# Optimization experiments

Measured on AMD Instinct MI355X. Metric: run time of the kernel, lower is better.

## Reference

```python
import jax, jax.numpy as jnp
import numpy as np

N, NFEAT, NFEAT_EXT, NHID, NCLASS, NHEADS = 8192, 512, 128, 256, 10, 8


def setup_inputs() -> dict:
    key = jax.random.key(0)
    ks = jax.random.split(key, 12)
    s = lambda fan_in: 1.0 / np.sqrt(fan_in)
    return {
        "x": jax.random.normal(ks[0], (N, NFEAT), jnp.float32),
        "adj": jax.random.uniform(ks[1], (N, N), jnp.float32) / N,  # row-stochastic-ish normalized adjacency
        "sub_fea": jax.random.normal(ks[2], (1, NFEAT_EXT), jnp.float32),
        # GraphConvolution 1: nfeat -> nhid
        "gc1_W": jax.random.normal(ks[3], (NFEAT, NHID), jnp.float32) * s(NFEAT),
        "gc1_b": jnp.zeros((NHID,), jnp.float32),
        # GraphConvolution 2: nhid -> 2*nhid
        "gc2_W": jax.random.normal(ks[4], (NHID, 2 * NHID), jnp.float32) * s(NHID),
        "gc2_b": jnp.zeros((2 * NHID,), jnp.float32),
        # fc1: nfeat_ext -> nhid
        "fc1_W": jax.random.normal(ks[5], (NFEAT_EXT, NHID), jnp.float32) * s(NFEAT_EXT),
        "fc1_b": jnp.zeros((NHID,), jnp.float32),
        # AttentionLayer(3*nhid, nclass, nheads): per-head projection + softmax head gating
        "att_W": jax.random.normal(ks[6], (NHEADS, 3 * NHID, NCLASS), jnp.float32) * s(3 * NHID),
        "att_a": jax.random.normal(ks[7], (NHEADS, 3 * NHID), jnp.float32) * s(3 * NHID),
        "att_b": jnp.zeros((NCLASS,), jnp.float32),
    }


def reference(x, adj, sub_fea, gc1_W, gc1_b, gc2_W, gc2_b, fc1_W, fc1_b, att_W, att_a, att_b):
    # GCN layer 1: adj @ (x @ W) + b, then ReLU
    h = jax.nn.relu(adj @ (x @ gc1_W) + gc1_b)            # [N, nhid]
    # GCN layer 2
    h = jax.nn.relu(adj @ (h @ gc2_W) + gc2_b)            # [N, 2*nhid]
    # global_mean_pool(batch=None): mean over all nodes -> single graph vector
    g = jax.nn.selu(jnp.mean(h, axis=0, keepdims=True))    # [1, 2*nhid]
    # dropout is identity in eval mode
    x_ext = sub_fea @ fc1_W + fc1_b                        # [1, nhid]
    z = jnp.concatenate([g, x_ext], axis=1)                # [1, 3*nhid]
    # multi-head attention fusion: softmax over head scores gating per-head projections
    scores = jnp.einsum("bi,hi->bh", z, att_a)            # [1, nheads]
    alpha = jax.nn.softmax(scores, axis=1)
    head_out = jnp.einsum("bi,hio->bho", z, att_W)        # [1, nheads, nclass]
    out = jnp.einsum("bh,bho->bo", alpha, head_out) + att_b  # [1, nclass]
    return jax.nn.log_softmax(out, axis=1)
```

## Files before the change

### kernel.cpp

```cpp
#include <hip/hip_runtime.h>

typedef __attribute__((ext_vector_type(8))) short short8;
typedef __attribute__((ext_vector_type(4))) float floatx4;
typedef unsigned short ushort_t;
typedef unsigned int u32;

__device__ __forceinline__ ushort_t f2bf(float x) {
  union { float f; unsigned int u; } v; v.f = x;
  unsigned int u = v.u;
  return (ushort_t)((u + 0x7FFFu + ((u >> 16) & 1u)) >> 16);
}
__device__ __forceinline__ unsigned int pk2(float a, float b) {
  return (unsigned int)f2bf(a) | ((unsigned int)f2bf(b) << 16);
}
__device__ __forceinline__ void gl_lds16(const void* g, void* l) {
  __builtin_amdgcn_global_load_lds(
      (const __attribute__((address_space(1))) u32*)g,
      (__attribute__((address_space(3))) u32*)l, 16, 0, 0);
}


__global__ void prep_t(const float* __restrict__ W1, const float* __restrict__ W2,
                       ushort_t* __restrict__ W1T, ushort_t* __restrict__ W2T) {
  int idx = blockIdx.x * 256 + threadIdx.x;
  int m = idx >> 9, k = idx & 511;
  W1T[((m >> 7) * 64 + (k >> 3)) * 1024 + (m & 127) * 8 + (k & 7)] = f2bf(W1[k * 256 + m]);
  int m2 = idx >> 8, k2 = idx & 255;
  W2T[((m2 >> 7) * 32 + (k2 >> 3)) * 1024 + (m2 & 127) * 8 + (k2 & 7)] = f2bf(W2[k2 * 512 + m2]);
}

__global__ __launch_bounds__(256) void tile_cvt(const float* __restrict__ src,
                                                ushort_t* __restrict__ dst, const int K) {
  __shared__ __align__(16) ushort_t ls[33024];
  const int t = threadIdx.x;
  const int rb = blockIdx.y, cb = blockIdx.x;
  const long sbase = (long)rb * 128 * K + cb * 256;
#pragma unroll 4
  for (int i = 0; i < 32; ++i) {
    int flat = i * 256 + t;
    int row = flat >> 6, kq = flat & 63;
    float4 v = *(const float4*)(src + sbase + (long)row * K + kq * 4);
    *(uint2*)(ls + ((kq >> 1) * 129 + row) * 8 + (kq & 1) * 4) =
        make_uint2(pk2(v.x, v.y), pk2(v.z, v.w));
  }
  __syncthreads();
  ushort_t* ob = dst + ((long)rb * (K >> 3) + cb * 32) * 1024;
  const uint4* lv = (const uint4*)ls;
  uint4* ov = (uint4*)ob;
#pragma unroll 4
  for (int i = 0; i < 16; ++i) {
    int o = i * 256 + t;
    ov[o] = lv[(o >> 7) * 129 + (o & 127)];
  }
}

template<int MT, int NT, int EPI>
__global__ __launch_bounds__(256, 2)
void gemm_t(const ushort_t* __restrict__ A, const ushort_t* __restrict__ B,
            const float* __restrict__ bias, float* __restrict__ Cf,
            float* __restrict__ gacc, const int K, const int N) {
  constexpr int MF = MT / 32, NF = NT / 32;
  constexpr int nA = MT / 64, nB = NT / 64;
  __shared__ __align__(16) ushort_t Als[MT * 32];
  __shared__ __align__(16) ushort_t Bls[NT * 32];

  const int t = threadIdx.x;
  const int lane = t & 63, w = t >> 6;
  const int wm = w >> 1, wn = w & 1;
  const int ml = lane & 15, quad = lane >> 4;
  const int m0 = blockIdx.y * MT, n0 = blockIdx.x * NT;
  const int Kper = K / gridDim.z, kbeg = blockIdx.z * Kper;

  const char* Ag = (const char*)(A + ((long)((m0 / MT) * (K >> 3) + (kbeg >> 3)) * MT) * 8);
  const char* Bg = (const char*)(B + ((long)((n0 / NT) * (K >> 3) + (kbeg >> 3)) * NT) * 8);

  floatx4 acc[MF][NF] = {};
  const int iters = Kper >> 5;
  for (int it = 0; it < iters; ++it) {
    __syncthreads();
#pragma unroll
    for (int c = 0; c < nA; ++c)
      gl_lds16(Ag + c * 4096 + t * 16, (char*)Als + c * 4096 + t * 16);
#pragma unroll
    for (int c = 0; c < nB; ++c)
      gl_lds16(Bg + c * 4096 + t * 16, (char*)Bls + c * 4096 + t * 16);
    Ag += MT * 64; Bg += NT * 64;
    __syncthreads();

    short8 av[MF], bv[NF];
#pragma unroll
    for (int f = 0; f < MF; ++f)
      av[f] = *(const short8*)(Als + (quad * MT + wm * (MT / 2) + f * 16 + ml) * 8);
#pragma unroll
    for (int f = 0; f < NF; ++f)
      bv[f] = *(const short8*)(Bls + (quad * NT + wn * (NT / 2) + f * 16 + ml) * 8);
#pragma unroll
    for (int fm = 0; fm < MF; ++fm)
#pragma unroll
      for (int fn = 0; fn < NF; ++fn)
        acc[fm][fn] = __builtin_amdgcn_mfma_f32_16x16x32_bf16(av[fm], bv[fn], acc[fm][fn], 0, 0, 0);
  }

  if constexpr (EPI == 2) {
#pragma unroll
    for (int fm = 0; fm < MF; ++fm) {
      int rowb = m0 + wm * (MT / 2) + fm * 16 + quad * 4;
#pragma unroll
      for (int r = 0; r < 4; ++r) {
        float bb = bias[rowb + r];
        float s = 0.f;
#pragma unroll
        for (int fn = 0; fn < NF; ++fn)
          s += fmaxf(acc[fm][fn][r] + bb, 0.f);
        s += __shfl_xor(s, 1);
        s += __shfl_xor(s, 2);
        s += __shfl_xor(s, 4);
        s += __shfl_xor(s, 8);
        if (ml == 0) atomicAdd(gacc + rowb + r, s);
      }
    }
  } else {
    const long zoff = (long)blockIdx.z * (long)gridDim.y * MT * N;
#pragma unroll
    for (int fm = 0; fm < MF; ++fm)
#pragma unroll
      for (int fn = 0; fn < NF; ++fn) {
        int gm = m0 + wm * (MT / 2) + fm * 16 + quad * 4;
        int gn = n0 + wn * (NT / 2) + fn * 16 + ml;
#pragma unroll
        for (int r = 0; r < 4; ++r)
          Cf[zoff + (long)(gm + r) * N + gn] = acc[fm][fn][r];
      }
  }
}

template<bool RELU_BIAS, int MAP>
__global__ void reduceZ(const float* __restrict__ p, ushort_t* __restrict__ outp,
                        const float* __restrict__ bias, const long total4,
                        const long zstride, const int Z) {
  long i = (long)blockIdx.x * blockDim.x + threadIdx.x;
  if (i >= total4) return;
  long e = i * 4;
  float4 s = *(const float4*)(p + e);
  for (int z = 1; z < Z; ++z) {
    float4 b = *(const float4*)(p + (long)z * zstride + e);
    s.x += b.x; s.y += b.y; s.z += b.z; s.w += b.w;
  }
  int row, k;
  if constexpr (MAP == 0) { row = (int)(e >> 13); k = (int)(e & 8191); }
  else                    { row = (int)(e >> 8);  k = (int)(e & 255);  }
  if constexpr (RELU_BIAS) {
    float bb = bias[row];
    s.x = fmaxf(s.x + bb, 0.f); s.y = fmaxf(s.y + bb, 0.f);
    s.z = fmaxf(s.z + bb, 0.f); s.w = fmaxf(s.w + bb, 0.f);
  }
  long o;
  if constexpr (MAP == 0) o = (long)(k >> 3) * 2048 + row * 8 + (k & 7);
  else                    o = (long)(row >> 7) * 32768 + (long)(k >> 3) * 1024 + (row & 127) * 8 + (k & 7);
  *(uint2*)(outp + o) = make_uint2(pk2(s.x, s.y), pk2(s.z, s.w));
}

__global__ void tail_kernel(const float* __restrict__ gacc, const float* __restrict__ sub_fea,
                            const float* __restrict__ fc1_W, const float* __restrict__ fc1_b,
                            const float* __restrict__ att_W, const float* __restrict__ att_a,
                            const float* __restrict__ att_b, float* __restrict__ out) {
  __shared__ float z[768];
  __shared__ float sc[8];
  __shared__ float alpha[8];
  __shared__ float outsh[10];
  const int t = threadIdx.x;

  for (int j = t; j < 512; j += 256) {
    float x = gacc[j] * (1.0f / 8192.0f);
    const float scale = 1.0507009873554805f, al = 1.6732632423543772f;
    z[j] = x > 0.f ? scale * x : scale * al * (expf(x) - 1.0f);
  }
  {
    float a = fc1_b[t];
    for (int i = 0; i < 128; ++i) a += sub_fea[i] * fc1_W[i * 256 + t];
    z[512 + t] = a;
  }
  if (t < 10) outsh[t] = 0.f;
  __syncthreads();

  {
    int h = t >> 5, ln = t & 31;
    float p = 0.f;
    for (int i = ln; i < 768; i += 32) p += z[i] * att_a[h * 768 + i];
    for (int m = 16; m; m >>= 1) p += __shfl_down(p, m, 32);
    if (ln == 0) sc[h] = p;
  }
  __syncthreads();
  if (t == 0) {
    float mx = sc[0];
    for (int h = 1; h < 8; ++h) mx = fmaxf(mx, sc[h]);
    float s = 0.f, e[8];
    for (int h = 0; h < 8; ++h) { e[h] = expf(sc[h] - mx); s += e[h]; }
    for (int h = 0; h < 8; ++h) alpha[h] = e[h] / s;
  }
  __syncthreads();

  float p[10];
#pragma unroll
  for (int o = 0; o < 10; ++o) p[o] = 0.f;
  for (int i = t; i < 768; i += 256) {
    float zi = z[i];
    for (int h = 0; h < 8; ++h) {
      float za = zi * alpha[h];
      const float* wp = att_W + (h * 768 + i) * 10;
#pragma unroll
      for (int o = 0; o < 10; ++o) p[o] += za * wp[o];
    }
  }
#pragma unroll
  for (int o = 0; o < 10; ++o) atomicAdd(&outsh[o], p[o]);
  __syncthreads();
  if (t == 0) {
    float v[10], mx = -1e30f;
    for (int o = 0; o < 10; ++o) { v[o] = outsh[o] + att_b[o]; mx = fmaxf(mx, v[o]); }
    float s = 0.f;
    for (int o = 0; o < 10; ++o) s += expf(v[o] - mx);
    float lse = logf(s) + mx;
    for (int o = 0; o < 10; ++o) out[o] = v[o] - lse;
  }
}

extern "C" void kernel_launch(void* const* d_in, const int* in_sizes, int n_in,
                              void* d_out, int out_size, void* d_ws, size_t ws_size,
                              hipStream_t stream) {
  const float* x       = (const float*)d_in[0];
  const float* adj     = (const float*)d_in[1];
  const float* sub_fea = (const float*)d_in[2];
  const float* gc1_W   = (const float*)d_in[3];
  const float* gc1_b   = (const float*)d_in[4];
  const float* gc2_W   = (const float*)d_in[5];
  const float* gc2_b   = (const float*)d_in[6];
  const float* fc1_W   = (const float*)d_in[7];
  const float* fc1_b   = (const float*)d_in[8];
  const float* att_W   = (const float*)d_in[9];
  const float* att_a   = (const float*)d_in[10];
  const float* att_b   = (const float*)d_in[11];
  float* out = (float*)d_out;

  const size_t MB = 1u << 20;
  char* ws = (char*)d_ws;
  size_t off = 0;
  ushort_t* adjT = (ushort_t*)(ws + off); off += 128 * MB;
  ushort_t* xT   = (ushort_t*)(ws + off); off += 8 * MB;
  ushort_t* t1T  = (ushort_t*)(ws + off); off += 4 * MB;
  ushort_t* h1T  = (ushort_t*)(ws + off); off += 4 * MB;
  ushort_t* P_t  = (ushort_t*)(ws + off); off += 4 * MB;
  float*    part = (float*)   (ws + off); off += 64 * MB;
  ushort_t* W1T  = (ushort_t*)(ws + off); off += 262144;
  ushort_t* W2T  = (ushort_t*)(ws + off); off += 262144;
  float*    gacc = (float*)   (ws + off);

  hipMemsetAsync(gacc, 0, 512 * sizeof(float), stream);
  prep_t<<<512, 256, 0, stream>>>(gc1_W, gc2_W, W1T, W2T);

  tile_cvt<<<dim3(32, 64), 256, 0, stream>>>(adj, adjT, 8192);
  tile_cvt<<<dim3(2, 64), 256, 0, stream>>>(x, xT, 512);

  gemm_t<128, 128, 3><<<dim3(64, 2, 2), 256, 0, stream>>>(W1T, xT, nullptr, part, nullptr, 512, 8192);
  reduceZ<false, 0><<<2048, 256, 0, stream>>>(part, t1T, nullptr, 524288L, 2097152L, 2);

  gemm_t<256, 128, 3><<<dim3(64, 1, 8), 256, 0, stream>>>(t1T, adjT, nullptr, part, nullptr, 8192, 8192);
  reduceZ<true, 0><<<2048, 256, 0, stream>>>(part, h1T, gc1_b, 524288L, 2097152L, 8);

  gemm_t<128, 256, 3><<<dim3(1, 64, 8), 256, 0, stream>>>(adjT, h1T, nullptr, part, nullptr, 8192, 256);
  reduceZ<false, 1><<<2048, 256, 0, stream>>>(part, P_t, nullptr, 524288L, 2097152L, 8);

  gemm_t<128, 128, 2><<<dim3(64, 4, 1), 256, 0, stream>>>(W2T, P_t, gc2_b, nullptr, gacc, 256, 8192);

  tail_kernel<<<1, 256, 0, stream>>>(gacc, sub_fea, fc1_W, fc1_b, att_W, att_a, att_b, out);
}
```

Before: 630.5 us.

## Store split-K partials in fragment-native layout and drop first-GEMM reduction

The split-K GEMMs now write fp32 partials in the accumulator's fragment order, so each wave writes contiguous 64-lane runs instead of scattered row-major elements. New dedicated reduce kernels remap those fragment slots back into the blocked bf16 layouts. The small x@W1 GEMM no longer uses split-K: it writes bf16 directly in the transposed blocked layout, which removes one partial buffer round-trip and one kernel launch. The cost is complex index arithmetic in the reducers, and less parallelism for the first GEMM.

```diff
diff --git a/kernel.cpp b/kernel.cpp
--- a/kernel.cpp
+++ b/kernel.cpp
@@ -119,45 +119,74 @@
         if (ml == 0) atomicAdd(gacc + rowb + r, s);
       }
     }
+  } else if constexpr (EPI == 3) {
+    const int tv = (NT == 256) ? blockIdx.y : blockIdx.x;
+    float* base = Cf + ((long)blockIdx.z * 64 + tv) * 32768 + (w * MF * NF * 4) * 64 + lane;
+#pragma unroll
+    for (int fm = 0; fm < MF; ++fm)
+#pragma unroll
+      for (int fn = 0; fn < NF; ++fn)
+#pragma unroll
+        for (int r = 0; r < 4; ++r)
+          base[((fm * NF + fn) * 4 + r) * 64] = acc[fm][fn][r];
   } else {
-    const long zoff = (long)blockIdx.z * (long)gridDim.y * MT * N;
+    ushort_t* C = (ushort_t*)Cf;
 #pragma unroll
     for (int fm = 0; fm < MF; ++fm)
 #pragma unroll
       for (int fn = 0; fn < NF; ++fn) {
         int gm = m0 + wm * (MT / 2) + fm * 16 + quad * 4;
         int gn = n0 + wn * (NT / 2) + fn * 16 + ml;
+        long ob = (long)(gn >> 3) * 2048 + (gn & 7);
 #pragma unroll
         for (int r = 0; r < 4; ++r)
-          Cf[zoff + (long)(gm + r) * N + gn] = acc[fm][fn][r];
+          C[ob + (long)(gm + r) * 8] = f2bf(acc[fm][fn][r]);
       }
   }
 }
 
-template<bool RELU_BIAS, int MAP>
-__global__ void reduceZ(const float* __restrict__ p, ushort_t* __restrict__ outp,
-                        const float* __restrict__ bias, const long total4,
-                        const long zstride, const int Z) {
-  long i = (long)blockIdx.x * blockDim.x + threadIdx.x;
-  if (i >= total4) return;
-  long e = i * 4;
-  float4 s = *(const float4*)(p + e);
-  for (int z = 1; z < Z; ++z) {
-    float4 b = *(const float4*)(p + (long)z * zstride + e);
+__global__ void reduce_L1b(const float* __restrict__ p, ushort_t* __restrict__ h1T,
+                           const float* __restrict__ bias) {
+  long i = (long)blockIdx.x * 256 + threadIdx.x;
+  long o = i * 4;
+  int j0 = (int)(o & 7);
+  int row = (int)((o >> 3) & 255);
+  int kc = (int)(o >> 11);
+  int k0 = kc * 8 + j0;
+  int tx = k0 >> 7, c0 = k0 & 127;
+  int wm = row >> 7, fm = (row >> 4) & 7, quad = (row >> 2) & 3, r = row & 3;
+  int wn = c0 >> 6, fn = (c0 >> 4) & 3, ml = c0 & 15;
+  int slot = ((((wm * 2 + wn) * 8 + fm) * 4 + fn) * 4 + r) * 64 + quad * 16 + ml;
+  const float* src = p + (long)tx * 32768 + slot;
+  float4 s = *(const float4*)src;
+  for (int z = 1; z < 8; ++z) {
+    float4 b = *(const float4*)(src + (long)z * 2097152);
     s.x += b.x; s.y += b.y; s.z += b.z; s.w += b.w;
   }
-  int row, k;
-  if constexpr (MAP == 0) { row = (int)(e >> 13); k = (int)(e & 8191); }
-  else                    { row = (int)(e >> 8);  k = (int)(e & 255);  }
-  if constexpr (RELU_BIAS) {
-    float bb = bias[row];
-    s.x = fmaxf(s.x + bb, 0.f); s.y = fmaxf(s.y + bb, 0.f);
-    s.z = fmaxf(s.z + bb, 0.f); s.w = fmaxf(s.w + bb, 0.f);
-  }
-  long o;
-  if constexpr (MAP == 0) o = (long)(k >> 3) * 2048 + row * 8 + (k & 7);
-  else                    o = (long)(row >> 7) * 32768 + (long)(k >> 3) * 1024 + (row & 127) * 8 + (k & 7);
-  *(uint2*)(outp + o) = make_uint2(pk2(s.x, s.y), pk2(s.z, s.w));
+  float bb = bias[row];
+  s.x = fmaxf(s.x + bb, 0.f); s.y = fmaxf(s.y + bb, 0.f);
+  s.z = fmaxf(s.z + bb, 0.f); s.w = fmaxf(s.w + bb, 0.f);
+  *(uint2*)(h1T + o) = make_uint2(pk2(s.x, s.y), pk2(s.z, s.w));
+}
+
+__global__ void reduce_L2a(const float* __restrict__ p, ushort_t* __restrict__ P_t) {
+  long i = (long)blockIdx.x * 256 + threadIdx.x;
+  long o = i * 4;
+  int j0 = (int)(o & 7);
+  int row = (int)((o >> 3) & 127);
+  int kc = (int)((o >> 10) & 31);
+  int ty = (int)(o >> 15);
+  int k0 = kc * 8 + j0;
+  int wm = row >> 6, fm = (row >> 4) & 3, quad = (row >> 2) & 3, r = row & 3;
+  int wn = k0 >> 7, fn = (k0 >> 4) & 7, ml = k0 & 15;
+  int slot = ((((wm * 2 + wn) * 4 + fm) * 8 + fn) * 4 + r) * 64 + quad * 16 + ml;
+  const float* src = p + (long)ty * 32768 + slot;
+  float4 s = *(const float4*)src;
+  for (int z = 1; z < 8; ++z) {
+    float4 b = *(const float4*)(src + (long)z * 2097152);
+    s.x += b.x; s.y += b.y; s.z += b.z; s.w += b.w;
+  }
+  *(uint2*)(P_t + o) = make_uint2(pk2(s.x, s.y), pk2(s.z, s.w));
 }
 
 __global__ void tail_kernel(const float* __restrict__ gacc, const float* __restrict__ sub_fea,
@@ -261,16 +290,19 @@
   tile_cvt<<<dim3(32, 64), 256, 0, stream>>>(adj, adjT, 8192);
   tile_cvt<<<dim3(2, 64), 256, 0, stream>>>(x, xT, 512);
 
-  gemm_t<128, 128, 3><<<dim3(64, 2, 2), 256, 0, stream>>>(W1T, xT, nullptr, part, nullptr, 512, 8192);
-  reduceZ<false, 0><<<2048, 256, 0, stream>>>(part, t1T, nullptr, 524288L, 2097152L, 2);
-
-  gemm_t<256, 128, 3><<<dim3(64, 1, 8), 256, 0, stream>>>(t1T, adjT, nullptr, part, nullptr, 8192, 8192);
-  reduceZ<true, 0><<<2048, 256, 0, stream>>>(part, h1T, gc1_b, 524288L, 2097152L, 8);
-
-  gemm_t<128, 256, 3><<<dim3(1, 64, 8), 256, 0, stream>>>(adjT, h1T, nullptr, part, nullptr, 8192, 256);
-  reduceZ<false, 1><<<2048, 256, 0, stream>>>(part, P_t, nullptr, 524288L, 2097152L, 8);
-
-  gemm_t<128, 128, 2><<<dim3(64, 4, 1), 256, 0, stream>>>(W2T, P_t, gc2_b, nullptr, gacc, 256, 8192);
+  gemm_t<128, 128, 4><<<dim3(64, 2, 1), 256, 0, stream>>>(
+      W1T, xT, nullptr, (float*)t1T, nullptr, 512, 8192);
+
+  gemm_t<256, 128, 3><<<dim3(64, 1, 8), 256, 0, stream>>>(
+      t1T, adjT, nullptr, part, nullptr, 8192, 8192);
+  reduce_L1b<<<2048, 256, 0, stream>>>(part, h1T, gc1_b);
+
+  gemm_t<128, 256, 3><<<dim3(1, 64, 8), 256, 0, stream>>>(
+      adjT, h1T, nullptr, part, nullptr, 8192, 256);
+  reduce_L2a<<<2048, 256, 0, stream>>>(part, P_t);
+
+  gemm_t<128, 128, 2><<<dim3(64, 4, 1), 256, 0, stream>>>(
+      W2T, P_t, gc2_b, nullptr, gacc, 256, 8192);
 
   tail_kernel<<<1, 256, 0, stream>>>(gacc, sub_fea, fc1_W, fc1_b, att_W, att_a, att_b, out);
 }
```

Result: slower. 644.3 us (+2.2%).
